# Kernel optimization log

Measured on AMD Instinct MI355X. Metric: run time of the kernel, lower is better.

## Reference

```python
import jax, jax.numpy as jnp
import numpy as np

N_, C_, H_, W_ = 8, 256, 64, 64
HEADS = 8
KS = 3
K2 = KS * KS
OUT = 256
HD = OUT // HEADS
STRIDE = 1
PAD = 1


def setup_inputs() -> dict:
    key = jax.random.key(0)
    ks = jax.random.split(key, 8)
    s = 0.05
    return {
        "input_features": jax.random.normal(ks[0], (N_, C_, H_, W_), jnp.float32),
        "Wq": jax.random.normal(ks[1], (OUT, C_), jnp.float32) * s,
        "Wk": jax.random.normal(ks[2], (OUT, C_), jnp.float32) * s,
        "Wv": jax.random.normal(ks[3], (OUT, C_), jnp.float32) * s,
        "off_w": jax.random.normal(ks[4], (HEADS * K2 * 2, C_, KS, KS), jnp.float32) * 0.01,
        "off_b": jnp.zeros((HEADS * K2 * 2,), jnp.float32),
        "attn_w": jax.random.normal(ks[5], (HEADS * K2, C_, KS, KS), jnp.float32) * 0.01,
        "attn_b": jnp.zeros((HEADS * K2,), jnp.float32),
        "Wo": jax.random.normal(ks[6], (OUT, OUT), jnp.float32) * s,
    }


def _conv2d(x, w, b):
    out = jax.lax.conv_general_dilated(
        x, w, (STRIDE, STRIDE), [(PAD, PAD), (PAD, PAD)],
        dimension_numbers=("NCHW", "OIHW", "NCHW"))
    return out + b[None, :, None, None]


def reference(input_features, Wq, Wk, Wv, off_w, off_b, attn_w, attn_b, Wo):
    x = input_features
    N, C, H, W = x.shape
    # query/key are projected but never used downstream in the original module
    q = jnp.einsum("oc,nchw->nohw", Wq, x)
    k = jnp.einsum("oc,nchw->nohw", Wk, x)
    v = jnp.einsum("oc,nchw->nohw", Wv, x)  # [N, OUT, H, W]

    offsets = _conv2d(x, off_w, off_b)                       # [N, HEADS*K2*2, Ho, Wo]
    aw = jax.nn.sigmoid(_conv2d(x, attn_w, attn_b))          # [N, HEADS*K2, Ho, Wo]
    Ho, Wo_sp = offsets.shape[2], offsets.shape[3]

    gx_base = jnp.linspace(-1.0, 1.0, Wo_sp)
    gy_base = jnp.linspace(-1.0, 1.0, Ho)

    # per-head, per-point (x,y) offsets, scaled by 2/[W,H] as in the source
    off = offsets.reshape(N, HEADS, K2, 2, Ho, Wo_sp)
    gx = gx_base[None, None, None, None, :] + off[:, :, :, 0] * (2.0 / W)  # [N,H,K2,Ho,Wo]
    gy = gy_base[None, None, None, :, None] + off[:, :, :, 1] * (2.0 / H)

    # grid_sample bilinear, align_corners=True, padding_mode='zeros'
    xp = (gx + 1.0) * 0.5 * (W - 1)
    yp = (gy + 1.0) * 0.5 * (H - 1)
    x0 = jnp.floor(xp).astype(jnp.int32)
    y0 = jnp.floor(yp).astype(jnp.int32)
    x1 = x0 + 1
    y1 = y0 + 1
    wx1 = xp - x0
    wx0 = 1.0 - wx1
    wy1 = yp - y0
    wy0 = 1.0 - wy1

    vf = v.reshape(N, HEADS, HD, H * W)

    def corner(yi, xi, wgt):
        valid = ((yi >= 0) & (yi < H) & (xi >= 0) & (xi < W)).astype(v.dtype)
        idx = (jnp.clip(yi, 0, H - 1) * W + jnp.clip(xi, 0, W - 1)).reshape(N, HEADS, -1)
        g = jnp.take_along_axis(vf, idx[:, :, None, :], axis=3)
        g = g.reshape(N, HEADS, HD, K2, Ho, Wo_sp)
        return g * (wgt * valid)[:, :, None]

    sampled = (corner(y0, x0, wy0 * wx0) + corner(y0, x1, wy0 * wx1)
               + corner(y1, x0, wy1 * wx0) + corner(y1, x1, wy1 * wx1))

    awr = aw.reshape(N, HEADS, K2, Ho, Wo_sp)
    head_out = jnp.einsum("nhckxy,nhkxy->nhcxy", sampled, awr)  # weighted sum over K2 points
    combined = head_out.reshape(N, OUT, Ho, Wo_sp)
    return jnp.einsum("oc,nchw->nohw", Wo, combined)
```

## Files before the change

kernel.cpp:

```cpp
#include <hip/hip_runtime.h>
#include <math.h>

#define N_    8
#define C_    256
#define H_    64
#define W_    64
#define HW    4096
#define OUT_  256
#define HEADS 8
#define HD    32
#define K2    9
#define OFFCH 144
#define AWCH  72
#define KTOT  2304
#define WPROWS 256
#define ABASE 16896

typedef __bf16 bf16x8 __attribute__((ext_vector_type(8)));
typedef __bf16 bf16x4 __attribute__((ext_vector_type(4)));
typedef float  f32x4  __attribute__((ext_vector_type(4)));

__device__ __forceinline__ void gload_lds16(const void* g, void* l) {
  __builtin_amdgcn_global_load_lds(
      (const __attribute__((address_space(1))) void*)g,
      (__attribute__((address_space(3))) void*)l, 16, 0, 0);
}

__device__ __forceinline__ void conv_body(
    __bf16* smem, const __bf16* __restrict__ xp, const __bf16* __restrict__ Wp,
    const float* __restrict__ biasp, const __bf16* __restrict__ zbuf,
    __bf16* __restrict__ P2, int yt, int bn, int n, int tid)
{
  const int y0 = yt << 1;
  const int lw = tid & 63, wv = tid >> 6;
  const int lr = lw & 15, lg = lw >> 4;

  f32x4 acc[8][2];
#pragma unroll
  for (int m = 0; m < 8; ++m)
#pragma unroll
    for (int nt = 0; nt < 2; ++nt) acc[m][nt] = (f32x4){0.f, 0.f, 0.f, 0.f};

  if (tid < 64) {
    int p = tid & 3, cs = (tid >> 2) & 1, r = (tid >> 3) & 3, buf = tid >> 5;
    int col = cs ? 65 : 0;
    *(uint4*)&smem[((buf * 4 + r) * 66 + col) * 32 + p * 8] =
        make_uint4(0u, 0u, 0u, 0u);
  }

  int aoff[3][4];
#pragma unroll
  for (int d = 0; d < 3; ++d)
#pragma unroll
    for (int mm = 0; mm < 4; ++mm) {
      int col = (mm << 4) + lr + d;
      int p = lg ^ ((col >> 1) & 3);
      aoff[d][mm] = col * 32 + p * 8;
    }
  int boff[2];
#pragma unroll
  for (int nt = 0; nt < 2; ++nt) {
    int col = (nt << 4) + lr;
    int p = lg ^ ((col >> 1) & 3);
    boff[nt] = ABASE + wv * 3072 + col * 32 + p * 8;
  }

  const int scg = lw & 3;
  const __bf16* gB[2];
#pragma unroll
  for (int jj = 0; jj < 2; ++jj) {
    int col = (jj << 4) + (lw >> 2);
    int cg = scg ^ ((col >> 1) & 3);
    gB[jj] = Wp + (size_t)(bn * 128 + wv * 32 + col) * KTOT + (cg << 3);
  }
  const __bf16* gA[4];
  int aAdd;
  {
    int y = y0 - 1 + wv;
    bool valid = ((unsigned)y < (unsigned)H_);
    aAdd = valid ? 1 : 0;
#pragma unroll
    for (int k = 0; k < 4; ++k) {
      int col = 1 + (k << 4) + (lw >> 2);
      int cg = scg ^ ((col >> 1) & 3);
      gA[k] = valid
          ? xp + ((size_t)(n * HW) + y * W_ + (col - 1)) * C_ + (cg << 3)
          : zbuf;
    }
  }

  auto stageB = [&](int elemOff, int pbuf) {
#pragma unroll
    for (int jj = 0; jj < 2; ++jj)
      gload_lds16(gB[jj] + elemOff,
                  &smem[ABASE + wv * 3072 + pbuf * 1024 + (jj << 9)]);
  };
  auto stageA = [&](int c0elem, int buf) {
    const int add = aAdd ? c0elem : 0;
#pragma unroll
    for (int k = 0; k < 4; ++k)
      gload_lds16(gA[k] + add,
                  &smem[((buf * 4 + wv) * 66 + 1 + (k << 4)) * 32]);
  };

  stageA(0, 0);
  stageB(0 * C_ + 0, 0);
  stageB(3 * C_ + 0, 1);
  asm volatile("s_waitcnt vmcnt(4)" ::: "memory");
  __builtin_amdgcn_s_barrier();
  asm volatile("" ::: "memory");

  for (int cc = 0; cc < 4; ++cc) {
    const bool lastcc = (cc == 3);
#pragma unroll
    for (int sub = 0; sub < 2; ++sub) {
      const int ci = (cc << 1) + sub;
      const int abuf = sub;
      bf16x8 a[8];
#pragma unroll
      for (int s = 0; s < 9; ++s) {
        const int dxp = s / 3, dy = s % 3;
        const int pbR = s % 3;
        const int pbW = (s + 2) % 3;
        const bool lastSlice = lastcc && (sub == 1);

        if (s == 1 && ci < 7) stageA((ci + 1) << 5, sub ^ 1);

        if (!(lastSlice && s >= 7)) {
          const int sn  = (s + 2 < 9) ? (s + 2) : (s - 7);
          const int cin = (s + 2 < 9) ? ci : (ci + 1);
          const int tn  = (sn % 3) * 3 + (sn / 3);
          stageB(tn * C_ + (cin << 5), pbW);
        }

        if (lastSlice && s == 8)
          asm volatile("s_waitcnt vmcnt(0)" ::: "memory");
        else if (lastSlice && s == 7)
          asm volatile("s_waitcnt vmcnt(2)" ::: "memory");
        else if ((s == 1 || s == 2) && ci < 7)
          asm volatile("s_waitcnt vmcnt(8)" ::: "memory");
        else
          asm volatile("s_waitcnt vmcnt(4)" ::: "memory");

        if (dy == 0) {
#pragma unroll
          for (int m = 0; m < 8; ++m) {
            const int rr = (m >> 2);
            a[m] = *(const bf16x8*)&smem[aoff[dxp][m & 3] +
                                         (abuf * 4 + rr) * 2112];
          }
        } else {
#pragma unroll
          for (int m = 0; m < 4; ++m) a[m] = a[m + 4];
#pragma unroll
          for (int m = 4; m < 8; ++m) {
            const int rr = 1 + dy;
            a[m] = *(const bf16x8*)&smem[aoff[dxp][m & 3] +
                                         (abuf * 4 + rr) * 2112];
          }
        }
        bf16x8 b[2];
#pragma unroll
        for (int nt = 0; nt < 2; ++nt)
          b[nt] = *(const bf16x8*)&smem[boff[nt] + (pbR << 10)];

        __builtin_amdgcn_s_setprio(1);
#pragma unroll
        for (int m = 0; m < 8; ++m)
#pragma unroll
          for (int nt = 0; nt < 2; ++nt)
            acc[m][nt] = __builtin_amdgcn_mfma_f32_16x16x32_bf16(
                a[m], b[nt], acc[m][nt], 0, 0, 0);
        __builtin_amdgcn_s_setprio(0);

        if (s == 8 && !lastSlice) {
          __builtin_amdgcn_s_barrier();
          asm volatile("" ::: "memory");
        }
      }
    }
  }

#pragma unroll
  for (int nt = 0; nt < 2; ++nt) {
    const int co = bn * 128 + wv * 32 + (nt << 4) + lr;
    if (co < 216) {
      const float bias = biasp[co];
      int idx;
      if (co < OFFCH) {
        int hh = co / 18;
        idx = (hh << 5) + (co - 18 * hh);
      } else {
        int r = co - OFFCH;
        int hh = r / 9;
        idx = (hh << 5) + 18 + (r - 9 * hh);
      }
#pragma unroll
      for (int m = 0; m < 8; ++m) {
#pragma unroll
        for (int reg = 0; reg < 4; ++reg) {
          const int sl = (m << 4) + (lg << 2) + reg;
          const int yout = y0 + (sl >> 6), xo = sl & 63;
          float v = acc[m][nt][reg] + bias;
          if (co >= OFFCH) v = 1.f / (1.f + expf(-v));
          P2[((size_t)n * HW + yout * W_ + xo) * 256 + idx] = (__bf16)v;
        }
      }
    }
  }
}

template <int MODE>
__device__ __forceinline__ void gemm_body(
    __bf16* smem, const __bf16* __restrict__ A, const __bf16* __restrict__ Wb,
    __bf16* __restrict__ out_b, float* __restrict__ out_f,
    int st, int bn, int n, int tid)
{
  const int s0 = st << 7;
  const int lw = tid & 63, wv = tid >> 6;
  const int lr = lw & 15, lg = lw >> 4;
  const int sm_base = wv << 5;

  f32x4 acc[2][8];
#pragma unroll
  for (int m = 0; m < 2; ++m)
#pragma unroll
    for (int nt = 0; nt < 8; ++nt) acc[m][nt] = (f32x4){0.f, 0.f, 0.f, 0.f};

  int aoff[2];
#pragma unroll
  for (int m = 0; m < 2; ++m) {
    int row = sm_base + (m << 4) + lr;
    int p = lg ^ ((row >> 1) & 3);
    aoff[m] = row * 32 + p * 8;
  }
  int boff[8];
#pragma unroll
  for (int nt = 0; nt < 8; ++nt) {
    int row = (nt << 4) + lr;
    int p = lg ^ ((row >> 1) & 3);
    boff[nt] = 12288 + row * 32 + p * 8;
  }

  const __bf16* gA[2];
  const __bf16* gB[2];
#pragma unroll
  for (int jj = 0; jj < 2; ++jj) {
    int j = wv * 2 + jj;
    int row = (j << 4) + (lw >> 2);
    int cg = (lw & 3) ^ ((row >> 1) & 3);
    gA[jj] = A + ((size_t)n * HW + s0 + row) * 256 + (cg << 3);
    gB[jj] = Wb + ((size_t)((bn << 7) + row)) * 256 + (cg << 3);
  }

  auto stage = [&](int k, int buf) {
    const int koff = k << 5;
#pragma unroll
    for (int jj = 0; jj < 2; ++jj)
      gload_lds16(gA[jj] + koff, &smem[buf * 4096 + ((wv * 2 + jj) << 9)]);
#pragma unroll
    for (int jj = 0; jj < 2; ++jj)
      gload_lds16(gB[jj] + koff,
                  &smem[12288 + buf * 4096 + ((wv * 2 + jj) << 9)]);
  };

  stage(0, 0);
  stage(1, 1);

#pragma unroll
  for (int k = 0; k < 8; ++k) {
    if (k < 7)
      asm volatile("s_waitcnt vmcnt(4)" ::: "memory");
    else
      asm volatile("s_waitcnt vmcnt(0)" ::: "memory");
    __builtin_amdgcn_s_barrier();
    asm volatile("" ::: "memory");

    if (k + 2 < 8) stage(k + 2, (k + 2) % 3);

    const int buf = k % 3;
    bf16x8 a[2], b[8];
#pragma unroll
    for (int m = 0; m < 2; ++m)
      a[m] = *(const bf16x8*)&smem[aoff[m] + buf * 4096];
#pragma unroll
    for (int nt = 0; nt < 8; ++nt)
      b[nt] = *(const bf16x8*)&smem[boff[nt] + buf * 4096];

    __builtin_amdgcn_s_setprio(1);
#pragma unroll
    for (int m = 0; m < 2; ++m)
#pragma unroll
      for (int nt = 0; nt < 8; ++nt)
        acc[m][nt] = __builtin_amdgcn_mfma_f32_16x16x32_bf16(
            a[m], b[nt], acc[m][nt], 0, 0, 0);
    __builtin_amdgcn_s_setprio(0);
  }

#pragma unroll
  for (int m = 0; m < 2; ++m) {
#pragma unroll
    for (int nt = 0; nt < 8; ++nt) {
      const int co = (bn << 7) + (nt << 4) + lr;
      if (MODE == 0) {
#pragma unroll
        for (int reg = 0; reg < 4; ++reg) {
          const int sm = sm_base + (m << 4) + (lg << 2) + reg;
          out_b[((size_t)n * HW + s0 + sm) * 256 + co] = (__bf16)acc[m][nt][reg];
        }
      } else {
        const int sm = sm_base + (m << 4) + (lg << 2);
        float4 v4 = make_float4(acc[m][nt][0], acc[m][nt][1],
                                acc[m][nt][2], acc[m][nt][3]);
        *(float4*)&out_f[((size_t)(n * 256 + co)) * HW + s0 + sm] = v4;
      }
    }
  }
}

__global__ __launch_bounds__(256) void fused_pre_kernel(
    const float* __restrict__ x, __bf16* __restrict__ xp,
    const float* __restrict__ off_w, const float* __restrict__ off_b,
    const float* __restrict__ attn_w, const float* __restrict__ attn_b,
    const float* __restrict__ Wv, const float* __restrict__ Wo,
    __bf16* __restrict__ Wp, float* __restrict__ biasp,
    __bf16* __restrict__ zbuf, __bf16* __restrict__ Wvb,
    __bf16* __restrict__ Wob)
{
  const int b = blockIdx.x;
  const int tid = threadIdx.x;
  __shared__ float tile[64][65];

  if (b < 2048) {
    const int c0 = (b & 3) << 6;
    const int y  = (b >> 2) & 63;
    const int n  = b >> 8;
    const int tx = tid & 63, tg = tid >> 6;
#pragma unroll
    for (int i = 0; i < 16; ++i) {
      int cl = tg + (i << 2);
      tile[cl][tx] = x[((size_t)(n * C_ + c0 + cl) * H_ + y) * W_ + tx];
    }
    __syncthreads();
#pragma unroll
    for (int i = 0; i < 16; ++i) {
      int xl = tg + (i << 2);
      xp[((size_t)(n * HW) + y * W_ + xl) * C_ + c0 + tx] = (__bf16)tile[tx][xl];
    }
  } else {
    const int bb = b - 2048;
    const int c = tid;
    if (bb < 256) {
      const int co = bb;
      if (co == 0) {
        *(uint4*)&zbuf[(size_t)c * 8] = make_uint4(0u, 0u, 0u, 0u);
      }
      const float* base = nullptr;
      if (co < OFFCH)      base = off_w  + ((size_t)co * C_ + c) * 9;
      else if (co < 216)   base = attn_w + ((size_t)(co - OFFCH) * C_ + c) * 9;
#pragma unroll
      for (int t = 0; t < 9; ++t) {
        float w = base ? base[t] : 0.f;
        Wp[(size_t)co * KTOT + t * C_ + c] = (__bf16)w;
      }
      if (c == 0) {
        float bv = 0.f;
        if (co < OFFCH) bv = off_b[co];
        else if (co < 216) bv = attn_b[co - OFFCH];
        biasp[co] = bv;
      }
    } else if (bb < 512) {
      const int i = (bb - 256) * 256 + c;
      Wvb[i] = (__bf16)Wv[i];
    } else {
      const int i = (bb - 512) * 256 + c;
      Wob[i] = (__bf16)Wo[i];
    }
  }
}

__global__ __launch_bounds__(256) void fused_cv_kernel(
    const __bf16* __restrict__ xp, const __bf16* __restrict__ Wp,
    const float* __restrict__ biasp, const __bf16* __restrict__ zbuf,
    __bf16* __restrict__ P2, const __bf16* __restrict__ Wvb,
    __bf16* __restrict__ vtb)
{
  __shared__ __align__(16) __bf16 smem[16896 + 12288];
  const int bn = blockIdx.y;
  if (bn < 2)
    conv_body(smem, xp, Wp, biasp, zbuf, P2, blockIdx.x, bn, blockIdx.z,
              threadIdx.x);
  else
    gemm_body<0>(smem, xp, Wvb, vtb, nullptr, blockIdx.x, bn - 2, blockIdx.z,
                 threadIdx.x);
}

__global__ __launch_bounds__(256) void wo_kernel(
    const __bf16* __restrict__ comb, const __bf16* __restrict__ Wob,
    float* __restrict__ out)
{
  __shared__ __align__(16) __bf16 smem[24576];
  gemm_body<1>(smem, comb, Wob, nullptr, out, blockIdx.x, blockIdx.y,
               blockIdx.z, threadIdx.x);
}

__global__ __launch_bounds__(256) void sample_kernel(
    const __bf16* __restrict__ vtb, const __bf16* __restrict__ P2,
    __bf16* __restrict__ comb)
{
  const int b = blockIdx.x;
  const int y = b & 63;
  const int h = (b >> 6) & 7;
  const int n = b >> 9;
  const int tid = threadIdx.x;
  const int xq = tid >> 2, cg = tid & 3;
  const int lw = tid & 63, wv = tid >> 6;

  __shared__ __align__(16) __bf16 vsl[8 * 64 * 32];

  const int xs = (wv << 4) + (lw >> 2);
  const int cs = lw & 3;
  const __bf16* vrow0 =
      vtb + ((size_t)n * HW) * 256 + (h << 5) + (cs << 3) + (size_t)xs * 256;
#pragma unroll
  for (int r = 0; r < 8; ++r) {
    int yy = y - 3 + r;
    if ((unsigned)yy < (unsigned)H_)
      gload_lds16(vrow0 + (size_t)yy * (64 * 256),
                  &vsl[(r * 64 + (wv << 4)) * 32]);
  }

  const __bf16* prow = P2 + ((size_t)n * HW + y * 64 + xq) * 256 + (h << 5);
  bf16x8 p0 = *(const bf16x8*)(prow);
  bf16x8 p1 = *(const bf16x8*)(prow + 8);
  bf16x8 p2 = *(const bf16x8*)(prow + 16);
  bf16x4 p3 = *(const bf16x4*)(prow + 24);

  __syncthreads();

  float acc[8];
#pragma unroll
  for (int j = 0; j < 8; ++j) acc[j] = 0.f;

  const __bf16* vbase = vtb + ((size_t)n * HW) * 256 + (h << 5) + (cg << 3);

#pragma unroll
  for (int k = 0; k < K2; ++k) {
    float offx, offy, a;
    if (k < 4)      { offx = (float)p0[2 * k];       offy = (float)p0[2 * k + 1]; }
    else if (k < 8) { offx = (float)p1[2 * (k - 4)]; offy = (float)p1[2 * (k - 4) + 1]; }
    else            { offx = (float)p2[0];           offy = (float)p2[1]; }
    if (k < 6)      a = (float)p2[2 + k];
    else            a = (float)p3[k - 6];

    const float xpf = (float)xq + offx * (63.f / 64.f);
    const float ypf = (float)y  + offy * (63.f / 64.f);
    const float fx0 = floorf(xpf), fy0 = floorf(ypf);
    const int x0 = (int)fx0, y0 = (int)fy0;
    const float wx1 = xpf - fx0, wx0 = 1.f - wx1;
    const float wy1 = ypf - fy0, wy0 = 1.f - wy1;

#pragma unroll
    for (int cy = 0; cy < 2; ++cy) {
      const int yi = y0 + cy;
      if ((unsigned)yi >= (unsigned)H_) continue;
      const float wy = cy ? wy1 : wy0;
      const int ridx = yi - (y - 3);
#pragma unroll
      for (int cx = 0; cx < 2; ++cx) {
        const int xi = x0 + cx;
        if ((unsigned)xi >= (unsigned)W_) continue;
        const float cw = a * wy * (cx ? wx1 : wx0);
        bf16x8 v;
        if ((unsigned)ridx < 8u) {
          v = *(const bf16x8*)&vsl[(ridx * 64 + xi) * 32 + (cg << 3)];
        } else {
          v = *(const bf16x8*)(vbase + (size_t)(yi * W_ + xi) * 256);
        }
#pragma unroll
        for (int j = 0; j < 8; ++j) acc[j] = fmaf(cw, (float)v[j], acc[j]);
      }
    }
  }

  bf16x8 r;
#pragma unroll
  for (int j = 0; j < 8; ++j) r[j] = (__bf16)acc[j];
  *(bf16x8*)&comb[((size_t)n * HW + y * 64 + xq) * 256 + (h << 5) + (cg << 3)] = r;
}

extern "C" void kernel_launch(void* const* d_in, const int* in_sizes, int n_in,
                              void* d_out, int out_size, void* d_ws,
                              size_t ws_size, hipStream_t stream)
{
  const float* x      = (const float*)d_in[0];
  const float* Wv     = (const float*)d_in[3];
  const float* off_w  = (const float*)d_in[4];
  const float* off_b  = (const float*)d_in[5];
  const float* attn_w = (const float*)d_in[6];
  const float* attn_b = (const float*)d_in[7];
  const float* Wo     = (const float*)d_in[8];
  float* out = (float*)d_out;

  __bf16* vtb   = (__bf16*)d_ws;
  __bf16* xp    = vtb + (size_t)N_ * HW * OUT_;
  __bf16* comb  = xp + (size_t)N_ * HW * C_;
  __bf16* P2    = comb + (size_t)N_ * HW * OUT_;
  __bf16* Wp    = P2 + (size_t)N_ * HW * 256;
  __bf16* Wvb   = Wp + (size_t)WPROWS * KTOT;
  __bf16* Wob   = Wvb + (size_t)OUT_ * C_;
  __bf16* zbuf  = Wob + (size_t)OUT_ * OUT_;
  float*  biasp = (float*)(zbuf + 2048);

  fused_pre_kernel<<<dim3(2816), 256, 0, stream>>>(
      x, xp, off_w, off_b, attn_w, attn_b, Wv, Wo, Wp, biasp, zbuf, Wvb, Wob);
  fused_cv_kernel<<<dim3(32, 4, N_), 256, 0, stream>>>(xp, Wp, biasp, zbuf, P2,
                                                       Wvb, vtb);
  sample_kernel<<<dim3(N_ * HEADS * H_), 256, 0, stream>>>(vtb, P2, comb);
  wo_kernel<<<dim3(32, 2, N_), 256, 0, stream>>>(comb, Wob, out);
}
```

Baseline: 111.5 us.

## Process two output rows per block in sampling kernel with 16 channels per thread

Each sample_kernel block now covers two output rows of one head instead of one. It stages a 9-row halo of V in LDS rather than 8 rows per single row, which roughly halves redundant halo loads per output row and halves the grid size. Each thread now handles 16 channels, so the bilinear coordinate and weight math is amortised over twice as many FMAs. The costs are more LDS, more registers per thread and fewer blocks to hide latency.

```diff
diff --git a/kernel.cpp b/kernel.cpp
--- a/kernel.cpp
+++ b/kernel.cpp
@@ -408,25 +408,28 @@
     const __bf16* __restrict__ vtb, const __bf16* __restrict__ P2,
     __bf16* __restrict__ comb)
 {
-  const int b = blockIdx.x;
-  const int y = b & 63;
-  const int h = (b >> 6) & 7;
-  const int n = b >> 9;
+  const int b  = blockIdx.x;
+  const int yp = b & 31;
+  const int h  = (b >> 5) & 7;
+  const int n  = b >> 8;
+  const int yb = yp << 1;
   const int tid = threadIdx.x;
-  const int xq = tid >> 2, cg = tid & 3;
-  const int lw = tid & 63, wv = tid >> 6;
-
-  __shared__ __align__(16) __bf16 vsl[8 * 64 * 32];
-
-  const int xs = (wv << 4) + (lw >> 2);
-  const int cs = lw & 3;
-  const __bf16* vrow0 =
+  const int cg  = tid & 1;
+  const int pt  = tid >> 1;
+  const int yloc = pt >> 6, xq = pt & 63;
+  const int y = yb + yloc;
+  const int wv = tid >> 6;
+
+  __shared__ __align__(16) __bf16 vsl[9 * 64 * 32];
+
+  const int xs = tid >> 2, cs = tid & 3;
+  const __bf16* vsrc =
       vtb + ((size_t)n * HW) * 256 + (h << 5) + (cs << 3) + (size_t)xs * 256;
 #pragma unroll
-  for (int r = 0; r < 8; ++r) {
-    int yy = y - 3 + r;
+  for (int r = 0; r < 9; ++r) {
+    int yy = yb - 3 + r;
     if ((unsigned)yy < (unsigned)H_)
-      gload_lds16(vrow0 + (size_t)yy * (64 * 256),
+      gload_lds16(vsrc + (size_t)yy * (64 * 256),
                   &vsl[(r * 64 + (wv << 4)) * 32]);
   }
 
@@ -438,11 +441,11 @@
 
   __syncthreads();
 
-  float acc[8];
-#pragma unroll
-  for (int j = 0; j < 8; ++j) acc[j] = 0.f;
-
-  const __bf16* vbase = vtb + ((size_t)n * HW) * 256 + (h << 5) + (cg << 3);
+  float acc[16];
+#pragma unroll
+  for (int j = 0; j < 16; ++j) acc[j] = 0.f;
+
+  const __bf16* vbase = vtb + ((size_t)n * HW) * 256 + (h << 5) + (cg << 4);
 
 #pragma unroll
   for (int k = 0; k < K2; ++k) {
@@ -456,37 +459,46 @@
     const float xpf = (float)xq + offx * (63.f / 64.f);
     const float ypf = (float)y  + offy * (63.f / 64.f);
     const float fx0 = floorf(xpf), fy0 = floorf(ypf);
-    const int x0 = (int)fx0, y0 = (int)fy0;
+    const int ix0 = (int)fx0, iy0 = (int)fy0;
     const float wx1 = xpf - fx0, wx0 = 1.f - wx1;
     const float wy1 = ypf - fy0, wy0 = 1.f - wy1;
 
 #pragma unroll
     for (int cy = 0; cy < 2; ++cy) {
-      const int yi = y0 + cy;
+      const int yi = iy0 + cy;
       if ((unsigned)yi >= (unsigned)H_) continue;
       const float wy = cy ? wy1 : wy0;
-      const int ridx = yi - (y - 3);
+      const int ridx = yi - (yb - 3);
 #pragma unroll
       for (int cx = 0; cx < 2; ++cx) {
-        const int xi = x0 + cx;
+        const int xi = ix0 + cx;
         if ((unsigned)xi >= (unsigned)W_) continue;
         const float cw = a * wy * (cx ? wx1 : wx0);
-        bf16x8 v;
-        if ((unsigned)ridx < 8u) {
-          v = *(const bf16x8*)&vsl[(ridx * 64 + xi) * 32 + (cg << 3)];
+        bf16x8 v0, v1;
+        if ((unsigned)ridx < 9u) {
+          const __bf16* lp = &vsl[(ridx * 64 + xi) * 32 + (cg << 4)];
+          v0 = *(const bf16x8*)lp;
+          v1 = *(const bf16x8*)(lp + 8);
         } else {
-          v = *(const bf16x8*)(vbase + (size_t)(yi * W_ + xi) * 256);
+          const __bf16* gp = vbase + (size_t)(yi * W_ + xi) * 256;
+          v0 = *(const bf16x8*)gp;
+          v1 = *(const bf16x8*)(gp + 8);
         }
 #pragma unroll
-        for (int j = 0; j < 8; ++j) acc[j] = fmaf(cw, (float)v[j], acc[j]);
-      }
-    }
-  }
-
-  bf16x8 r;
-#pragma unroll
-  for (int j = 0; j < 8; ++j) r[j] = (__bf16)acc[j];
-  *(bf16x8*)&comb[((size_t)n * HW + y * 64 + xq) * 256 + (h << 5) + (cg << 3)] = r;
+        for (int j = 0; j < 8; ++j) acc[j] = fmaf(cw, (float)v0[j], acc[j]);
+#pragma unroll
+        for (int j = 0; j < 8; ++j)
+          acc[8 + j] = fmaf(cw, (float)v1[j], acc[8 + j]);
+      }
+    }
+  }
+
+  bf16x8 r0, r1;
+#pragma unroll
+  for (int j = 0; j < 8; ++j) { r0[j] = (__bf16)acc[j]; r1[j] = (__bf16)acc[8 + j]; }
+  __bf16* crow = comb + ((size_t)n * HW + y * 64 + xq) * 256 + (h << 5) + (cg << 4);
+  *(bf16x8*)crow = r0;
+  *(bf16x8*)(crow + 8) = r1;
 }
 
 extern "C" void kernel_launch(void* const* d_in, const int* in_sizes, int n_in,
@@ -516,6 +528,6 @@
       x, xp, off_w, off_b, attn_w, attn_b, Wv, Wo, Wp, biasp, zbuf, Wvb, Wob);
   fused_cv_kernel<<<dim3(32, 4, N_), 256, 0, stream>>>(xp, Wp, biasp, zbuf, P2,
                                                        Wvb, vtb);
-  sample_kernel<<<dim3(N_ * HEADS * H_), 256, 0, stream>>>(vtb, P2, comb);
+  sample_kernel<<<dim3(N_ * HEADS * 32), 256, 0, stream>>>(vtb, P2, comb);
   wo_kernel<<<dim3(32, 2, N_), 256, 0, stream>>>(comb, Wob, out);
 }
```

Result: faster. 106.9 us, median of 2 (-4.2%).
